# Performance work log

Hardware: AMD Instinct MI355X
Metric: run time of the kernel (lower is better)

## Reference

```python
import jax, jax.numpy as jnp
import numpy as np
import math

B, S, I, C = 1, 256, 512, 256   # batch, msa rows, residues, c_s
H, D = 8, 32                     # num_heads, head_dim; total = H*D = 256
EPS = 1e-5


def setup_inputs() -> dict:
    key = jax.random.key(0)
    ks = jax.random.split(key, 10)
    s = 0.02
    return {
        "msa_representation": jax.random.normal(ks[0], (B, S, I, C), jnp.float32),
        "ln_gamma": jnp.ones((C,), jnp.float32),
        "ln_beta": jnp.zeros((C,), jnp.float32),
        # weights stored [in, out] (torch Linear applies x @ W.T; equivalent math)
        "Wq": jax.random.normal(ks[1], (C, H * D), jnp.float32) * s,
        "Wk": jax.random.normal(ks[2], (C, D), jnp.float32) * s,
        "Wv": jax.random.normal(ks[3], (C, D), jnp.float32) * s,
        "Wg": jax.random.normal(ks[4], (C, H * D), jnp.float32) * s,
        "bg": jnp.zeros((H * D,), jnp.float32),
        "Wo": jax.random.normal(ks[5], (H * D, C), jnp.float32) * s,
        "bo": jnp.zeros((C,), jnp.float32),
    }


def reference(msa_representation, ln_gamma, ln_beta, Wq, Wk, Wv, Wg, bg, Wo, bo):
    x = msa_representation
    mu = jnp.mean(x, axis=-1, keepdims=True)
    var = jnp.mean(jnp.square(x - mu), axis=-1, keepdims=True)
    x = (x - mu) * jax.lax.rsqrt(var + EPS) * ln_gamma + ln_beta  # [B,S,I,C]

    Q = (x @ Wq).reshape(B, S, I, H, D).mean(axis=1)              # [B,I,H,D]
    K = x @ Wk                                                    # [B,S,I,D] ('btid')
    V = x @ Wv                                                    # [B,S,I,D]
    G = jax.nn.sigmoid(x @ Wg + bg).reshape(B, S, I, H, D)        # [B,S,I,H,D]

    scores = jnp.einsum('bihd,btid->bhti', Q, K) / math.sqrt(D)   # [B,H,S,I]
    attn = jax.nn.softmax(scores, axis=-2)                        # softmax over rows t
    weighted = jnp.einsum('bhti,btid->bihd', attn, V)             # [B,I,H,D]

    values = (G * weighted[:, None]).reshape(B, S, I, H * D)
    return values @ Wo + bo                                       # [B,S,I,C]
```

## Files before the change

### kernel.cpp

```cpp
#include <hip/hip_runtime.h>
#include <hip/hip_bf16.h>

#define S_DIM 256
#define I_DIM 512
#define NROWS (S_DIM * I_DIM)

using bf16x8 = __attribute__((ext_vector_type(8))) short;
using f32x4  = __attribute__((ext_vector_type(4))) float;
typedef unsigned short ushort_t;

__device__ __forceinline__ unsigned short f2bf(float f) {
  unsigned int u = __builtin_bit_cast(unsigned int, f);
  u += 0x7fffu + ((u >> 16) & 1u);
  return (unsigned short)(u >> 16);
}
__device__ __forceinline__ float bf2f(unsigned short u) {
  unsigned int x = ((unsigned int)u) << 16;
  return __builtin_bit_cast(float, x);
}
__device__ __forceinline__ void gl_lds16(const void* g, void* l) {
  __builtin_amdgcn_global_load_lds(
      (const __attribute__((address_space(1))) void*)g,
      (__attribute__((address_space(3))) void*)l, 16, 0, 0);
}

__global__ __launch_bounds__(256) void prep_weights(
    const float* __restrict__ Wk, const float* __restrict__ Wv,
    const float* __restrict__ Wg, const float* __restrict__ Wo,
    ushort_t* __restrict__ WkvT, ushort_t* __restrict__ WgT,
    ushort_t* __restrict__ WoT) {
  int t = blockIdx.x * 256 + threadIdx.x;
  int n = t >> 8, c = t & 255;
  if (t < 64 * 256) {
    float v = (n < 32) ? Wk[c * 32 + n] : Wv[c * 32 + (n - 32)];
    WkvT[t] = f2bf(v);
  }
  WgT[t] = f2bf(Wg[c * 256 + n]);
  WoT[t] = f2bf(Wo[c * 256 + n]);
}

__global__ __launch_bounds__(256) void ln_kv_kernel(
    const float* __restrict__ x, const float* __restrict__ gamma,
    const float* __restrict__ beta, const ushort_t* __restrict__ WkvT,
    ushort_t* __restrict__ xn, float* __restrict__ xpart,
    ushort_t* __restrict__ KVb) {
  __shared__ float sacc[4][256];
  __shared__ __attribute__((aligned(16))) ushort_t xs[64 * 264];
  __shared__ __attribute__((aligned(16))) ushort_t wt[64 * 264];
  int b = blockIdx.x;
  int i = b & (I_DIM - 1);
  int sq = b >> 9;
  int tid = threadIdx.x;
  int w = tid >> 6;
  int lane = tid & 63;

  const uint4* wg_ = (const uint4*)WkvT;
#pragma unroll
  for (int j = 0; j < 8; ++j) {
    int idx = tid + j * 256;
    *(uint4*)(&wt[(idx >> 5) * 264 + (idx & 31) * 8]) = wg_[idx];
  }

  float4 gv = *(const float4*)(gamma + lane * 4);
  float4 bv = *(const float4*)(beta + lane * 4);
  float p0 = 0.f, p1 = 0.f, p2 = 0.f, p3 = 0.f;

#pragma unroll 4
  for (int it = 0; it < 16; ++it) {
    int s = sq * 64 + w * 16 + it;
    size_t row = (size_t)s * I_DIM + i;
    float4 xv = *(const float4*)(x + row * 256 + lane * 4);
    float sum = xv.x + xv.y + xv.z + xv.w;
    float sq2 = xv.x*xv.x + xv.y*xv.y + xv.z*xv.z + xv.w*xv.w;
#pragma unroll
    for (int off = 32; off >= 1; off >>= 1) {
      sum += __shfl_xor(sum, off);
      sq2 += __shfl_xor(sq2, off);
    }
    float mu = sum * (1.f / 256.f);
    float rs = rsqrtf(sq2 * (1.f / 256.f) - mu * mu + 1e-5f);
    float y0 = (xv.x - mu) * rs * gv.x + bv.x;
    float y1 = (xv.y - mu) * rs * gv.y + bv.y;
    float y2 = (xv.z - mu) * rs * gv.z + bv.z;
    float y3 = (xv.w - mu) * rs * gv.w + bv.w;
    ushort4 o;
    o.x = f2bf(y0); o.y = f2bf(y1); o.z = f2bf(y2); o.w = f2bf(y3);
    *(ushort4*)(xn + row * 256 + lane * 4) = o;
    *(ushort4*)(&xs[(w * 16 + it) * 264 + lane * 4]) = o;
    p0 += y0; p1 += y1; p2 += y2; p3 += y3;
  }
  sacc[w][lane * 4 + 0] = p0;
  sacc[w][lane * 4 + 1] = p1;
  sacc[w][lane * 4 + 2] = p2;
  sacc[w][lane * 4 + 3] = p3;
  __syncthreads();
  xpart[((size_t)sq * I_DIM + i) * 256 + tid] =
      sacc[0][tid] + sacc[1][tid] + sacc[2][tid] + sacc[3][tid];

  int m15 = lane & 15, q = lane >> 4;
  f32x4 acc[4] = {};
#pragma unroll
  for (int k = 0; k < 8; ++k) {
    bf16x8 a = *(const bf16x8*)(&xs[(w * 16 + m15) * 264 + k * 32 + q * 8]);
#pragma unroll
    for (int nt = 0; nt < 4; ++nt) {
      bf16x8 bb = *(const bf16x8*)(&wt[(nt * 16 + m15) * 264 + k * 32 + q * 8]);
      acc[nt] = __builtin_amdgcn_mfma_f32_16x16x32_bf16(a, bb, acc[nt], 0, 0, 0);
    }
  }
#pragma unroll
  for (int nt = 0; nt < 4; ++nt)
#pragma unroll
    for (int r = 0; r < 4; ++r) {
      int s = sq * 64 + w * 16 + q * 4 + r;
      KVb[((size_t)s * I_DIM + i) * 64 + nt * 16 + m15] = f2bf(acc[nt][r]);
    }
}

__global__ __launch_bounds__(256) void q_kernel(
    const float* __restrict__ xpart, const float* __restrict__ Wq,
    float* __restrict__ Q) {
  int i = blockIdx.x, col = threadIdx.x;
  __shared__ float xr[256];
  float s = xpart[((size_t)0 * I_DIM + i) * 256 + col]
          + xpart[((size_t)1 * I_DIM + i) * 256 + col]
          + xpart[((size_t)2 * I_DIM + i) * 256 + col]
          + xpart[((size_t)3 * I_DIM + i) * 256 + col];
  xr[col] = s * (1.f / 256.f);
  __syncthreads();
  float acc = 0.f;
#pragma unroll 8
  for (int c = 0; c < 256; ++c) acc = fmaf(xr[c], Wq[c * 256 + col], acc);
  Q[i * 256 + col] = acc * 0.17677669529663687f;
}

__global__ __launch_bounds__(256) void attn_kernel(
    const ushort_t* __restrict__ KVb, const float* __restrict__ Q,
    float* __restrict__ weighted) {
  __shared__ ushort_t Vs[256 * 36];
  __shared__ float sl[8 * 264];
  __shared__ float ql[256];
  int i = blockIdx.x, tid = threadIdx.x;

  ql[tid] = Q[i * 256 + tid];
  const uint4* src = (const uint4*)(KVb + ((size_t)tid * I_DIM + i) * 64);
  uint4 kr0 = src[0], kr1 = src[1], kr2 = src[2], kr3 = src[3];
#pragma unroll
  for (int j = 0; j < 4; ++j) {
    uint4 v = src[4 + j];
    *(ushort4*)(&Vs[tid * 36 + j * 8 + 0]) = *(ushort4*)&v.x;
    *(ushort4*)(&Vs[tid * 36 + j * 8 + 4]) = *(ushort4*)&v.z;
  }
  ushort_t ks[32];
  *(uint4*)&ks[0] = kr0; *(uint4*)&ks[8] = kr1;
  *(uint4*)&ks[16] = kr2; *(uint4*)&ks[24] = kr3;
  float kf[32];
#pragma unroll
  for (int d = 0; d < 32; ++d) kf[d] = bf2f(ks[d]);
  __syncthreads();

#pragma unroll
  for (int h = 0; h < 8; ++h) {
    float sc = 0.f;
#pragma unroll
    for (int d = 0; d < 32; ++d) sc = fmaf(kf[d], ql[h * 32 + d], sc);
    sl[h * 264 + tid] = sc;
  }
  __syncthreads();

  int w = tid >> 6, lane = tid & 63;
#pragma unroll
  for (int hh = 0; hh < 2; ++hh) {
    int h = w * 2 + hh;
    float v0 = sl[h * 264 + lane], v1 = sl[h * 264 + lane + 64];
    float v2 = sl[h * 264 + lane + 128], v3 = sl[h * 264 + lane + 192];
    float m = fmaxf(fmaxf(v0, v1), fmaxf(v2, v3));
#pragma unroll
    for (int off = 32; off >= 1; off >>= 1) m = fmaxf(m, __shfl_xor(m, off));
    float e0 = __expf(v0 - m), e1 = __expf(v1 - m);
    float e2 = __expf(v2 - m), e3 = __expf(v3 - m);
    float ssum = e0 + e1 + e2 + e3;
#pragma unroll
    for (int off = 32; off >= 1; off >>= 1) ssum += __shfl_xor(ssum, off);
    float inv = 1.f / ssum;
    sl[h * 264 + lane] = e0 * inv;
    sl[h * 264 + lane + 64] = e1 * inv;
    sl[h * 264 + lane + 128] = e2 * inv;
    sl[h * 264 + lane + 192] = e3 * inv;
  }
  __syncthreads();

  int h = tid >> 5, d = tid & 31;
  float acc = 0.f;
#pragma unroll 4
  for (int t = 0; t < 256; ++t)
    acc = fmaf(sl[h * 264 + t], bf2f(Vs[t * 36 + d]), acc);
  weighted[i * 256 + tid] = acc;
}

__global__ __launch_bounds__(512) void gate_out_kernel(
    const ushort_t* __restrict__ xn, const ushort_t* __restrict__ WgT,
    const ushort_t* __restrict__ WoT, const float* __restrict__ weighted,
    const float* __restrict__ bg, const float* __restrict__ bo,
    float* __restrict__ out) {
  __shared__ __attribute__((aligned(16))) ushort_t Ab[2][32 * 256];
  __shared__ __attribute__((aligned(16))) ushort_t valT[32 * 256];
  const int tid = threadIdx.x;
  const int w = tid >> 6, lane = tid & 63;
  const int m15 = lane & 15, q = lane >> 4;
  const size_t base = (size_t)blockIdx.x * 512;

  bf16x8 wgf[2][8], wof[2][8];
#pragma unroll
  for (int ct = 0; ct < 2; ++ct) {
    int n = w * 32 + ct * 16 + m15;
#pragma unroll
    for (int kk = 0; kk < 8; ++kk) {
      int ku = kk * 4 + q;
      wgf[ct][kk] = *(const bf16x8*)(WgT + (size_t)n * 256 + ku * 8);
      wof[ct][kk] = *(const bf16x8*)(WoT + (size_t)n * 256 + ku * 8);
    }
  }
  float4 bgv[2], bov[2];
#pragma unroll
  for (int ct = 0; ct < 2; ++ct) {
    int col0 = w * 32 + ct * 16 + q * 4;
    bgv[ct] = *(const float4*)(bg + col0);
    bov[ct] = *(const float4*)(bo + col0);
  }

#pragma unroll
  for (int it = 0; it < 2; ++it) {
    int L = it * 512 + tid;
    int r = L >> 5, u = L & 31;
    int us = (u & 24) | ((u & 7) ^ (r & 7));
    gl_lds16(xn + (base + r) * 256 + us * 8, &Ab[0][(it * 512 + w * 64) * 8]);
  }
  __syncthreads();

#pragma unroll 1
  for (int t = 0; t < 16; ++t) {
    const int cur = t & 1;
    if (t < 15) {
#pragma unroll
      for (int it = 0; it < 2; ++it) {
        int L = it * 512 + tid;
        int r = L >> 5, u = L & 31;
        int us = (u & 24) | ((u & 7) ^ (r & 7));
        gl_lds16(xn + (base + (size_t)(t + 1) * 32 + r) * 256 + us * 8,
                 &Ab[cur ^ 1][(it * 512 + w * 64) * 8]);
      }
    }

    f32x4 acc1[2][2];
    const f32x4 zero = {0.f, 0.f, 0.f, 0.f};
    acc1[0][0] = zero; acc1[0][1] = zero; acc1[1][0] = zero; acc1[1][1] = zero;
#pragma unroll
    for (int kk = 0; kk < 8; ++kk) {
      int ku = kk * 4 + q;
      int ub = (ku & 24) | ((ku & 7) ^ (m15 & 7));
      bf16x8 b0 = *(const bf16x8*)&Ab[cur][(0 * 16 + m15) * 256 + ub * 8];
      bf16x8 b1 = *(const bf16x8*)&Ab[cur][(1 * 16 + m15) * 256 + ub * 8];
#pragma unroll
      for (int ct = 0; ct < 2; ++ct) {
        acc1[ct][0] = __builtin_amdgcn_mfma_f32_16x16x32_bf16(wgf[ct][kk], b0, acc1[ct][0], 0, 0, 0);
        acc1[ct][1] = __builtin_amdgcn_mfma_f32_16x16x32_bf16(wgf[ct][kk], b1, acc1[ct][1], 0, 0, 0);
      }
    }

#pragma unroll
    for (int mt = 0; mt < 2; ++mt) {
      int rloc = mt * 16 + m15;
      int i = t * 32 + rloc;
#pragma unroll
      for (int ct = 0; ct < 2; ++ct) {
        int col0 = w * 32 + ct * 16 + q * 4;
        float4 wv = *(const float4*)(weighted + (size_t)i * 256 + col0);
        float pz0 = acc1[ct][mt][0] + bgv[ct].x;
        float pz1 = acc1[ct][mt][1] + bgv[ct].y;
        float pz2 = acc1[ct][mt][2] + bgv[ct].z;
        float pz3 = acc1[ct][mt][3] + bgv[ct].w;
        float g0 = 1.f / (1.f + __expf(-pz0));
        float g1 = 1.f / (1.f + __expf(-pz1));
        float g2 = 1.f / (1.f + __expf(-pz2));
        float g3 = 1.f / (1.f + __expf(-pz3));
        ushort4 o;
        o.x = f2bf(g0 * wv.x); o.y = f2bf(g1 * wv.y);
        o.z = f2bf(g2 * wv.z); o.w = f2bf(g3 * wv.w);
        int u = col0 >> 3;
        int us = (u & 24) | ((u & 7) ^ (rloc & 7));
        *(ushort4*)(&valT[rloc * 256 + us * 8 + (col0 & 7)]) = o;
      }
    }

    __builtin_amdgcn_sched_barrier(0);
    asm volatile("s_waitcnt lgkmcnt(0)" ::: "memory");
    __builtin_amdgcn_s_barrier();
    __builtin_amdgcn_sched_barrier(0);

    f32x4 acc2[2][2];
    acc2[0][0] = zero; acc2[0][1] = zero; acc2[1][0] = zero; acc2[1][1] = zero;
#pragma unroll
    for (int kk = 0; kk < 8; ++kk) {
      int ku = kk * 4 + q;
      int ub = (ku & 24) | ((ku & 7) ^ (m15 & 7));
      bf16x8 b0 = *(const bf16x8*)&valT[(0 * 16 + m15) * 256 + ub * 8];
      bf16x8 b1 = *(const bf16x8*)&valT[(1 * 16 + m15) * 256 + ub * 8];
#pragma unroll
      for (int ct = 0; ct < 2; ++ct) {
        acc2[ct][0] = __builtin_amdgcn_mfma_f32_16x16x32_bf16(wof[ct][kk], b0, acc2[ct][0], 0, 0, 0);
        acc2[ct][1] = __builtin_amdgcn_mfma_f32_16x16x32_bf16(wof[ct][kk], b1, acc2[ct][1], 0, 0, 0);
      }
    }

#pragma unroll
    for (int mt = 0; mt < 2; ++mt) {
      size_t row = base + (size_t)t * 32 + mt * 16 + m15;
#pragma unroll
      for (int ct = 0; ct < 2; ++ct) {
        int col0 = w * 32 + ct * 16 + q * 4;
        float4 ov;
        ov.x = acc2[ct][mt][0] + bov[ct].x;
        ov.y = acc2[ct][mt][1] + bov[ct].y;
        ov.z = acc2[ct][mt][2] + bov[ct].z;
        ov.w = acc2[ct][mt][3] + bov[ct].w;
        *(float4*)(out + row * 256 + col0) = ov;
      }
    }

    __syncthreads();
  }
}

extern "C" void kernel_launch(void* const* d_in, const int* in_sizes, int n_in,
                              void* d_out, int out_size, void* d_ws, size_t ws_size,
                              hipStream_t stream) {
  const float* msa = (const float*)d_in[0];
  const float* gam = (const float*)d_in[1];
  const float* bet = (const float*)d_in[2];
  const float* Wq  = (const float*)d_in[3];
  const float* Wk  = (const float*)d_in[4];
  const float* Wv  = (const float*)d_in[5];
  const float* Wg  = (const float*)d_in[6];
  const float* bg  = (const float*)d_in[7];
  const float* Wo  = (const float*)d_in[8];
  const float* bo  = (const float*)d_in[9];
  float* out = (float*)d_out;

  char* ws = (char*)d_ws;
  ushort_t* xn     = (ushort_t*)ws;
  float* xpart     = (float*)(ws + 67108864);
  float* Q         = (float*)(ws + 69206016);
  ushort_t* KVb    = (ushort_t*)(ws + 69730304);
  float* weighted  = (float*)(ws + 86507520);
  ushort_t* WkvT   = (ushort_t*)(ws + 87031808);
  ushort_t* WgT    = (ushort_t*)(ws + 87064576);
  ushort_t* WoT    = (ushort_t*)(ws + 87195648);

  prep_weights<<<256, 256, 0, stream>>>(Wk, Wv, Wg, Wo, WkvT, WgT, WoT);
  ln_kv_kernel<<<2048, 256, 0, stream>>>(msa, gam, bet, WkvT, xn, xpart, KVb);
  q_kernel<<<512, 256, 0, stream>>>(xpart, Wq, Q);
  attn_kernel<<<512, 256, 0, stream>>>(KVb, Q, weighted);
  gate_out_kernel<<<256, 512, 0, stream>>>(xn, WgT, WoT, weighted, bg, bo, out);
}
```

Before: 353.9 us.

## Halve gate_out rows per block and stream weight fragments to cut registers

The gate/output kernel now processes 256 rows per block over 512 blocks instead of 512 rows over 256 blocks, so more blocks are available to spread across CUs. The Wg and Wo fragments no longer sit in registers for the whole kernel. They share one buffer that is reloaded from global/L2 between the two GEMM phases, and launch_bounds(512,4) asks for higher occupancy. Each 32-row tile now reloads the weights (and the biases), adding L2 traffic and load latency in exchange for fewer VGPRs and more parallelism. The weighted-value loads are also hoisted ahead of the first GEMM.

```diff
diff --git a/kernel.cpp b/kernel.cpp
--- a/kernel.cpp
+++ b/kernel.cpp
@@ -198,7 +198,7 @@
   weighted[i * 256 + tid] = acc;
 }
 
-__global__ __launch_bounds__(512) void gate_out_kernel(
+__global__ __launch_bounds__(512, 4) void gate_out_kernel(
     const ushort_t* __restrict__ xn, const ushort_t* __restrict__ WgT,
     const ushort_t* __restrict__ WoT, const float* __restrict__ weighted,
     const float* __restrict__ bg, const float* __restrict__ bo,
@@ -208,26 +208,24 @@
   const int tid = threadIdx.x;
   const int w = tid >> 6, lane = tid & 63;
   const int m15 = lane & 15, q = lane >> 4;
-  const size_t base = (size_t)blockIdx.x * 512;
-
-  bf16x8 wgf[2][8], wof[2][8];
+  const size_t base = (size_t)blockIdx.x * 256;
+  const int i0 = (int)(base & (I_DIM - 1));
+
+  const ushort_t* wgp[2];
+  const ushort_t* wop[2];
 #pragma unroll
   for (int ct = 0; ct < 2; ++ct) {
     int n = w * 32 + ct * 16 + m15;
-#pragma unroll
-    for (int kk = 0; kk < 8; ++kk) {
-      int ku = kk * 4 + q;
-      wgf[ct][kk] = *(const bf16x8*)(WgT + (size_t)n * 256 + ku * 8);
-      wof[ct][kk] = *(const bf16x8*)(WoT + (size_t)n * 256 + ku * 8);
-    }
-  }
-  float4 bgv[2], bov[2];
-#pragma unroll
-  for (int ct = 0; ct < 2; ++ct) {
-    int col0 = w * 32 + ct * 16 + q * 4;
-    bgv[ct] = *(const float4*)(bg + col0);
-    bov[ct] = *(const float4*)(bo + col0);
-  }
+    wgp[ct] = WgT + (size_t)n * 256 + q * 8;
+    wop[ct] = WoT + (size_t)n * 256 + q * 8;
+  }
+
+  bf16x8 wbuf[2][8];
+#pragma unroll
+  for (int ct = 0; ct < 2; ++ct)
+#pragma unroll
+    for (int kk = 0; kk < 8; ++kk)
+      wbuf[ct][kk] = *(const bf16x8*)(wgp[ct] + kk * 32);
 
 #pragma unroll
   for (int it = 0; it < 2; ++it) {
@@ -239,9 +237,9 @@
   __syncthreads();
 
 #pragma unroll 1
-  for (int t = 0; t < 16; ++t) {
+  for (int t = 0; t < 8; ++t) {
     const int cur = t & 1;
-    if (t < 15) {
+    if (t < 7) {
 #pragma unroll
       for (int it = 0; it < 2; ++it) {
         int L = it * 512 + tid;
@@ -251,6 +249,16 @@
                  &Ab[cur ^ 1][(it * 512 + w * 64) * 8]);
       }
     }
+    float4 wv[2][2];
+#pragma unroll
+    for (int mt = 0; mt < 2; ++mt) {
+      int i = i0 + t * 32 + mt * 16 + m15;
+#pragma unroll
+      for (int ct = 0; ct < 2; ++ct) {
+        int col0 = w * 32 + ct * 16 + q * 4;
+        wv[mt][ct] = *(const float4*)(weighted + (size_t)i * 256 + col0);
+      }
+    }
 
     f32x4 acc1[2][2];
     const f32x4 zero = {0.f, 0.f, 0.f, 0.f};
@@ -263,30 +271,35 @@
       bf16x8 b1 = *(const bf16x8*)&Ab[cur][(1 * 16 + m15) * 256 + ub * 8];
 #pragma unroll
       for (int ct = 0; ct < 2; ++ct) {
-        acc1[ct][0] = __builtin_amdgcn_mfma_f32_16x16x32_bf16(wgf[ct][kk], b0, acc1[ct][0], 0, 0, 0);
-        acc1[ct][1] = __builtin_amdgcn_mfma_f32_16x16x32_bf16(wgf[ct][kk], b1, acc1[ct][1], 0, 0, 0);
-      }
-    }
+        acc1[ct][0] = __builtin_amdgcn_mfma_f32_16x16x32_bf16(wbuf[ct][kk], b0, acc1[ct][0], 0, 0, 0);
+        acc1[ct][1] = __builtin_amdgcn_mfma_f32_16x16x32_bf16(wbuf[ct][kk], b1, acc1[ct][1], 0, 0, 0);
+      }
+    }
+
+#pragma unroll
+    for (int ct = 0; ct < 2; ++ct)
+#pragma unroll
+      for (int kk = 0; kk < 8; ++kk)
+        wbuf[ct][kk] = *(const bf16x8*)(wop[ct] + kk * 32);
 
 #pragma unroll
     for (int mt = 0; mt < 2; ++mt) {
       int rloc = mt * 16 + m15;
-      int i = t * 32 + rloc;
 #pragma unroll
       for (int ct = 0; ct < 2; ++ct) {
         int col0 = w * 32 + ct * 16 + q * 4;
-        float4 wv = *(const float4*)(weighted + (size_t)i * 256 + col0);
-        float pz0 = acc1[ct][mt][0] + bgv[ct].x;
-        float pz1 = acc1[ct][mt][1] + bgv[ct].y;
-        float pz2 = acc1[ct][mt][2] + bgv[ct].z;
-        float pz3 = acc1[ct][mt][3] + bgv[ct].w;
+        float4 bgv = *(const float4*)(bg + col0);
+        float pz0 = acc1[ct][mt][0] + bgv.x;
+        float pz1 = acc1[ct][mt][1] + bgv.y;
+        float pz2 = acc1[ct][mt][2] + bgv.z;
+        float pz3 = acc1[ct][mt][3] + bgv.w;
         float g0 = 1.f / (1.f + __expf(-pz0));
         float g1 = 1.f / (1.f + __expf(-pz1));
         float g2 = 1.f / (1.f + __expf(-pz2));
         float g3 = 1.f / (1.f + __expf(-pz3));
         ushort4 o;
-        o.x = f2bf(g0 * wv.x); o.y = f2bf(g1 * wv.y);
-        o.z = f2bf(g2 * wv.z); o.w = f2bf(g3 * wv.w);
+        o.x = f2bf(g0 * wv[mt][ct].x); o.y = f2bf(g1 * wv[mt][ct].y);
+        o.z = f2bf(g2 * wv[mt][ct].z); o.w = f2bf(g3 * wv[mt][ct].w);
         int u = col0 >> 3;
         int us = (u & 24) | ((u & 7) ^ (rloc & 7));
         *(ushort4*)(&valT[rloc * 256 + us * 8 + (col0 & 7)]) = o;
@@ -308,10 +321,16 @@
       bf16x8 b1 = *(const bf16x8*)&valT[(1 * 16 + m15) * 256 + ub * 8];
 #pragma unroll
       for (int ct = 0; ct < 2; ++ct) {
-        acc2[ct][0] = __builtin_amdgcn_mfma_f32_16x16x32_bf16(wof[ct][kk], b0, acc2[ct][0], 0, 0, 0);
-        acc2[ct][1] = __builtin_amdgcn_mfma_f32_16x16x32_bf16(wof[ct][kk], b1, acc2[ct][1], 0, 0, 0);
-      }
-    }
+        acc2[ct][0] = __builtin_amdgcn_mfma_f32_16x16x32_bf16(wbuf[ct][kk], b0, acc2[ct][0], 0, 0, 0);
+        acc2[ct][1] = __builtin_amdgcn_mfma_f32_16x16x32_bf16(wbuf[ct][kk], b1, acc2[ct][1], 0, 0, 0);
+      }
+    }
+
+#pragma unroll
+    for (int ct = 0; ct < 2; ++ct)
+#pragma unroll
+      for (int kk = 0; kk < 8; ++kk)
+        wbuf[ct][kk] = *(const bf16x8*)(wgp[ct] + kk * 32);
 
 #pragma unroll
     for (int mt = 0; mt < 2; ++mt) {
@@ -319,11 +338,12 @@
 #pragma unroll
       for (int ct = 0; ct < 2; ++ct) {
         int col0 = w * 32 + ct * 16 + q * 4;
+        float4 bov = *(const float4*)(bo + col0);
         float4 ov;
-        ov.x = acc2[ct][mt][0] + bov[ct].x;
-        ov.y = acc2[ct][mt][1] + bov[ct].y;
-        ov.z = acc2[ct][mt][2] + bov[ct].z;
-        ov.w = acc2[ct][mt][3] + bov[ct].w;
+        ov.x = acc2[ct][mt][0] + bov.x;
+        ov.y = acc2[ct][mt][1] + bov.y;
+        ov.z = acc2[ct][mt][2] + bov.z;
+        ov.w = acc2[ct][mt][3] + bov.w;
         *(float4*)(out + row * 256 + col0) = ov;
       }
     }
@@ -361,5 +381,5 @@
   ln_kv_kernel<<<2048, 256, 0, stream>>>(msa, gam, bet, WkvT, xn, xpart, KVb);
   q_kernel<<<512, 256, 0, stream>>>(xpart, Wq, Q);
   attn_kernel<<<512, 256, 0, stream>>>(KVb, Q, weighted);
-  gate_out_kernel<<<256, 512, 0, stream>>>(xn, WgT, WoT, weighted, bg, bo, out);
-}
+  gate_out_kernel<<<512, 512, 0, stream>>>(xn, WgT, WoT, weighted, bg, bo, out);
+}
```

Result: slower. 440.3 us (+24.4%).
